# Performance work log

Measured on AMD Instinct MI355X. Metric: run time of the kernel, lower is better.

## Reference

```python
import jax, jax.numpy as jnp
import numpy as np

B = 32768
D_IN = 512      # input_dim == dict_dim (forced by the STE add)
HID = 512       # hard-coded hidden width of linear1
D = 512         # dict_dim / embedding_dim
P = 8           # per_factor_dict_size: number of codebooks / MLP branches
K = 10          # num_factor: codebook size (rows per embedding table)
COMMIT = 0.25


def setup_inputs() -> dict:
    key = jax.random.key(0)
    ks = jax.random.split(key, 7)
    s1 = 1.0 / np.sqrt(D_IN)
    s2 = 1.0 / np.sqrt(HID)
    return {
        "inputs": jax.random.normal(ks[0], (B, D_IN), jnp.float32),
        "W1": jax.random.uniform(ks[1], (P, HID, D_IN), jnp.float32, -s1, s1),
        "b1": jax.random.uniform(ks[2], (P, HID), jnp.float32, -s1, s1),
        "W2": jax.random.uniform(ks[3], (P, D, HID), jnp.float32, -s2, s2),
        "b2": jax.random.uniform(ks[4], (P, D), jnp.float32, -s2, s2),
        # embedding init: uniform(-1/num_factor, 1/num_factor)
        "E": jax.random.uniform(ks[5], (P, K, D), jnp.float32, -1.0 / K, 1.0 / K),
        "label_gen": jax.random.randint(ks[6], (B,), 0, K, jnp.int64),
    }


def reference(inputs, W1, b1, W2, b2, E, label_gen):
    sg = jax.lax.stop_gradient
    # P parallel 2-layer MLPs: [P, B, D]
    h = jax.nn.relu(jnp.einsum("bd,phd->pbh", inputs, W1) + b1[:, None, :])
    z = jnp.einsum("pbh,peh->pbe", h, W2) + b2[:, None, :]
    # squared-distance expansion per codebook: [P, B, K]
    distances = (
        jnp.sum(z * z, axis=-1, keepdims=True)
        + jnp.sum(E * E, axis=-1)[:, None, :]
        - 2.0 * jnp.einsum("pbd,pkd->pbk", z, E)
    )
    ave_distances = jnp.mean(distances, axis=0)          # [B, K]
    idx = jnp.argmin(ave_distances, axis=1)              # [B]
    # one-hot @ E[p] then mean over p == mean codebook gathered at idx
    Emean = jnp.mean(E, axis=0)                          # [K, D]
    vq = Emean[idx]                                      # [B, D]
    vq_z = inputs + sg(vq - inputs)                      # straight-through
    # all_vq_z[j] = mean_p E[p, j]; losses vs every code row: [K, B]
    diff1 = Emean[:, None, :] - sg(inputs)[None, :, :]   # [K, B, D]
    diff2 = sg(Emean)[:, None, :] - inputs[None, :, :]
    all_vq_loss = jnp.sum(diff1 * diff1, axis=-1) + COMMIT * jnp.sum(diff2 * diff2, axis=-1)
    all_vq_z = inputs[None, :, :] + sg(Emean[:, None, :] - inputs[None, :, :])  # [K, B, D]
    changed_vq_z = Emean[label_gen]                      # [B, D]
    return (vq_z, distances, all_vq_z, all_vq_loss, changed_vq_z)
```

## Files before the change

### kernel.cpp

```cpp
#include <hip/hip_runtime.h>
#include <stdint.h>

typedef _Float16 f16;
typedef _Float16 f16x4 __attribute__((ext_vector_type(4)));
typedef _Float16 f16x8 __attribute__((ext_vector_type(8)));
typedef float f32x4 __attribute__((ext_vector_type(4)));

#define B_ROWS 32768
#define DIM 512
#define NP 8
#define NK 10

typedef __attribute__((address_space(3))) unsigned int lds_u32;
typedef __attribute__((address_space(1))) const unsigned int gbl_u32;

__device__ __forceinline__ void gload_lds16(const void* g, void* l) {
  __builtin_amdgcn_global_load_lds((gbl_u32*)(uintptr_t)g, (lds_u32*)(uintptr_t)l, 16, 0, 0);
}


__global__ void prep_split(const float4* __restrict__ X4, f16x4* __restrict__ Xh4,
                           f16x4* __restrict__ Xl4, const float4* __restrict__ W14,
                           f16x4* __restrict__ W1h4, f16x4* __restrict__ W1l4,
                           const float4* __restrict__ W24, f16x4* __restrict__ W2h4) {
  int bid = blockIdx.x, tid = threadIdx.x;
  if (bid < 1024) {
    for (int i = bid * 256 + tid; i < 4194304; i += 1024 * 256) {
      float4 v = X4[i];
      f16x4 h = {(f16)v.x, (f16)v.y, (f16)v.z, (f16)v.w};
      f16x4 l = {(f16)(v.x - (float)h[0]), (f16)(v.y - (float)h[1]),
                 (f16)(v.z - (float)h[2]), (f16)(v.w - (float)h[3])};
      Xh4[i] = h;
      Xl4[i] = l;
    }
  } else if (bid < 1152) {
    for (int i = (bid - 1024) * 256 + tid; i < 524288; i += 128 * 256) {
      float4 v = W14[i];
      f16x4 h = {(f16)v.x, (f16)v.y, (f16)v.z, (f16)v.w};
      f16x4 l = {(f16)(v.x - (float)h[0]), (f16)(v.y - (float)h[1]),
                 (f16)(v.z - (float)h[2]), (f16)(v.w - (float)h[3])};
      W1h4[i] = h;
      W1l4[i] = l;
    }
  } else {
    for (int i = (bid - 1152) * 256 + tid; i < 524288; i += 128 * 256) {
      float4 v = W24[i];
      f16x4 h = {(f16)v.x, (f16)v.y, (f16)v.z, (f16)v.w};
      W2h4[i] = h;
    }
  }
}


__global__ void enorm2(const float* __restrict__ E, float* __restrict__ Emean,
                       float* __restrict__ E2, float* __restrict__ E2m) {
  int bid = blockIdx.x;
  int lane = threadIdx.x;
  if (bid < 80) {
    const float* src = E + (size_t)bid * DIM;
    float s = 0.f;
    for (int i = lane; i < DIM; i += 64) {
      float v = src[i];
      s = fmaf(v, v, s);
    }
#pragma unroll
    for (int m = 1; m < 64; m <<= 1) s += __shfl_xor(s, m, 64);
    if (lane == 0) E2[bid] = s;
  } else {
    int k = bid - 80;
    float acc = 0.f;
    for (int i = lane; i < DIM; i += 64) {
      float s = 0.f;
#pragma unroll
      for (int p = 0; p < NP; ++p) s += E[p * NK * DIM + k * DIM + i];
      s *= 0.125f;
      Emean[k * DIM + i] = s;
      acc = fmaf(s, s, acc);
    }
#pragma unroll
    for (int m = 1; m < 64; m <<= 1) acc += __shfl_xor(acc, m, 64);
    if (lane == 0) E2m[k] = acc;
  }
}


__global__ __launch_bounds__(512) void etilde_kernel(const float* __restrict__ W2,
                                                     const float* __restrict__ b2,
                                                     const float* __restrict__ E,
                                                     f16* __restrict__ EimgH,
                                                     f16* __restrict__ EimgL,
                                                     float* __restrict__ c_) {
  const int p = blockIdx.x / NK, k = blockIdx.x % NK;
  const int h = threadIdx.x;
  __shared__ float Er[512];
  __shared__ float red[8];
  Er[h] = E[((size_t)p * NK + k) * DIM + h];
  __syncthreads();
  const float* Wp = W2 + (size_t)p * DIM * DIM;
  float s = 0.f;
#pragma unroll 8
  for (int d = 0; d < DIM; ++d) s = fmaf(Wp[(size_t)d * DIM + h], Er[d], s);
  int ei = p * 8320 + k * 520 + h;
  f16 hi = (f16)s;
  EimgH[ei] = hi;
  EimgL[ei] = (f16)(s - (float)hi);
  if (h < 8) {
    int pi = p * 8320 + k * 520 + 512 + h;
    EimgH[pi] = (f16)0.f;
    EimgL[pi] = (f16)0.f;
  }
  if (k == 0) {
    for (int j = h; j < 6 * 520; j += 512) {
      int pi = p * 8320 + 10 * 520 + j;
      EimgH[pi] = (f16)0.f;
      EimgL[pi] = (f16)0.f;
    }
  }
  float t = b2[p * DIM + h] * Er[h];
#pragma unroll
  for (int m = 1; m < 64; m <<= 1) t += __shfl_xor(t, m, 64);
  if ((h & 63) == 0) red[h >> 6] = t;
  __syncthreads();
  if (h == 0) {
    float cc = 0.f;
#pragma unroll
    for (int i = 0; i < 8; ++i) cc += red[i];
    c_[p * NK + k] = cc;
  }
}


template <int NBN, int GRP>
__global__ __launch_bounds__(256) void gemm1_k32(
    const f16* __restrict__ Ah_, const f16* __restrict__ Al_,
    const f16* __restrict__ Bh_, const f16* __restrict__ Bl_,
    const float* __restrict__ bias_,
    f16* __restrict__ Oh, f16* __restrict__ Ol, int ldo) {
  __shared__ f16 smem[32768];
  const int tid = threadIdx.x;
  const int lane = tid & 63;
  const int wave = tid >> 6;
  const int wr = wave >> 1, wc = wave & 1;

  const int q8 = gridDim.x >> 3;
  const int bid = blockIdx.x;
  const int swz = (bid & 7) * q8 + (bid >> 3);
  const int band = swz / (GRP * NBN);
  const int r_ = swz % (GRP * NBN);
  const int bm = band * GRP + (r_ % GRP);
  const int bn = r_ / GRP;
  const int m0 = bm * 128, n0 = bn * 128;

  f32x4 acc[4][4] = {};

  auto stage = [&](int buf, int s) {
    int k0 = s * 32;
    f16* base = smem + buf * 16384;
#pragma unroll
    for (int rnd = 0; rnd < 2; ++rnd) {
      int w = rnd * 256 + tid;
      int r = w >> 2;
      int c = ((w & 3) ^ ((r >> 1) & 3)) * 8;
      gload_lds16(Ah_ + (size_t)(m0 + r) * 512 + k0 + c, base + (size_t)w * 8);
      gload_lds16(Al_ + (size_t)(m0 + r) * 512 + k0 + c, base + 4096 + (size_t)w * 8);
      gload_lds16(Bh_ + (size_t)(n0 + r) * 512 + k0 + c, base + 8192 + (size_t)w * 8);
      gload_lds16(Bl_ + (size_t)(n0 + r) * 512 + k0 + c, base + 12288 + (size_t)w * 8);
    }
  };

  stage(0, 0);
  __syncthreads();

  const int g = lane >> 4, rl = lane & 15;

  for (int s = 0; s < 16; ++s) {
    if (s + 1 < 16) stage((s + 1) & 1, s + 1);
    const char* base = (const char*)(smem + (s & 1) * 16384);
    f16x8 af[4][2], bf[4][2];
#pragma unroll
    for (int i = 0; i < 4; ++i) {
      int ra = wr * 64 + i * 16 + rl;
      int offa = ra * 64 + ((g ^ ((ra >> 1) & 3)) << 4);
      af[i][0] = *(const f16x8*)(base + offa);
      af[i][1] = *(const f16x8*)(base + 8192 + offa);
      int rb = wc * 64 + i * 16 + rl;
      int offb = rb * 64 + ((g ^ ((rb >> 1) & 3)) << 4);
      bf[i][0] = *(const f16x8*)(base + 16384 + offb);
      bf[i][1] = *(const f16x8*)(base + 24576 + offb);
    }
#pragma unroll
    for (int i = 0; i < 4; ++i)
#pragma unroll
      for (int jn = 0; jn < 4; ++jn) {
        acc[i][jn] = __builtin_amdgcn_mfma_f32_16x16x32_f16(af[i][0], bf[jn][0], acc[i][jn], 0, 0, 0);
        acc[i][jn] = __builtin_amdgcn_mfma_f32_16x16x32_f16(af[i][0], bf[jn][1], acc[i][jn], 0, 0, 0);
        acc[i][jn] = __builtin_amdgcn_mfma_f32_16x16x32_f16(af[i][1], bf[jn][0], acc[i][jn], 0, 0, 0);
      }
    __syncthreads();
  }

#pragma unroll
  for (int jn = 0; jn < 4; ++jn) {
    int cg = n0 + wc * 64 + jn * 16 + rl;
    float bv = bias_[cg];
#pragma unroll
    for (int i = 0; i < 4; ++i) {
      int r0 = m0 + wr * 64 + i * 16 + g * 4;
#pragma unroll
      for (int r = 0; r < 4; ++r) {
        float z = acc[i][jn][r] + bv;
        z = fmaxf(z, 0.f);
        f16 h = (f16)z;
        size_t off = (size_t)(r0 + r) * ldo + cg;
        Oh[off] = h;
        Ol[off] = (f16)(z - (float)h);
      }
    }
  }
}


__global__ __launch_bounds__(256) void g2d_union(
    const f16* __restrict__ Hh, const f16* __restrict__ Hl,
    const f16* __restrict__ W2h, const float* __restrict__ b2,
    const f16* __restrict__ EimgH, const f16* __restrict__ EimgL,
    const float* __restrict__ c_, float* __restrict__ part2,
    float* __restrict__ gout) {
  __shared__ char pool[66048];
  const int tid = threadIdx.x;
  const int p = blockIdx.y;

  if (blockIdx.x < 1024) {
    f16* smem = (f16*)pool;
    const int lane = tid & 63, wave = tid >> 6;
    const int wr = wave >> 1, wc = wave & 1;
    const int bid = blockIdx.x;
    const int swz = (bid & 7) * 128 + (bid >> 3);
    const int bm = swz >> 2, bn = swz & 3;
    const int m0 = bm * 128, n0 = bn * 128;
    const f16* Ahp = Hh + (size_t)p * 512;
    const f16* Bhp = W2h + (size_t)p * 262144;

    f32x4 acc[4][4] = {};

    auto stage = [&](int buf, int t) {
      int k0 = t * 64;
      f16* sA = smem + buf * 16384;
      f16* sB = sA + 8192;
#pragma unroll
      for (int j = 0; j < 4; ++j) {
        int r = j * 32 + (tid >> 3);
        int c = ((tid & 7) ^ (r & 7)) * 8;
        gload_lds16(Ahp + (size_t)(m0 + r) * 4096 + k0 + c, sA + j * 2048 + tid * 8);
        gload_lds16(Bhp + (size_t)(n0 + r) * 512 + k0 + c, sB + j * 2048 + tid * 8);
      }
    };

    stage(0, 0);
    __syncthreads();
    const int g = lane >> 4, rl = lane & 15;
    for (int s = 0; s < 8; ++s) {
      if (s + 1 < 8) stage((s + 1) & 1, s + 1);
      const char* sA = (const char*)(smem + (s & 1) * 16384);
      const char* sB = sA + 16384;
      f16x8 af[4][2], bf[4][2];
#pragma unroll
      for (int i = 0; i < 4; ++i) {
        int ra = wr * 64 + i * 16 + rl;
        int rb = wc * 64 + i * 16 + rl;
#pragma unroll
        for (int kk = 0; kk < 2; ++kk) {
          int cb = kk * 64 + g * 16;
          af[i][kk] = *(const f16x8*)(sA + ra * 128 + (cb ^ ((ra & 7) << 4)));
          bf[i][kk] = *(const f16x8*)(sB + rb * 128 + (cb ^ ((rb & 7) << 4)));
        }
      }
#pragma unroll
      for (int i = 0; i < 4; ++i)
#pragma unroll
        for (int jn = 0; jn < 4; ++jn)
#pragma unroll
          for (int kk = 0; kk < 2; ++kk)
            acc[i][jn] = __builtin_amdgcn_mfma_f32_16x16x32_f16(af[i][kk], bf[jn][kk], acc[i][jn], 0, 0, 0);
      __syncthreads();
    }

    const float* bp = b2 + (size_t)p * 512;
    float bvals[4];
#pragma unroll
    for (int jn = 0; jn < 4; ++jn) bvals[jn] = bp[n0 + wc * 64 + jn * 16 + rl];
    const int ch = bn * 2 + wc;
    float* pb = part2 + (size_t)(p * 8 + ch) * B_ROWS;
#pragma unroll
    for (int i = 0; i < 4; ++i) {
#pragma unroll
      for (int r = 0; r < 4; ++r) {
        float q = 0.f;
#pragma unroll
        for (int jn = 0; jn < 4; ++jn) {
          float z = acc[i][jn][r] + bvals[jn];
          q = fmaf(z, z, q);
        }
#pragma unroll
        for (int m = 1; m < 16; m <<= 1) q += __shfl_xor(q, m, 64);
        if (rl == 0) pb[m0 + wr * 64 + i * 16 + g * 4 + r] = q;
      }
    }
  } else {
    f16* sH = (f16*)pool;
    f16* sL = (f16*)(pool + 16384);
    f16* sEh = (f16*)(pool + 32768);
    f16* sEl = (f16*)(pool + 49408);
    const int lane = tid & 63, wave = tid >> 6;
    const int r0 = (blockIdx.x - 1024) * 64;
    {
      const uint32_t* ih = (const uint32_t*)(EimgH + (size_t)p * 16 * 520);
      const uint32_t* il = (const uint32_t*)(EimgL + (size_t)p * 16 * 520);
      uint32_t* oh = (uint32_t*)sEh;
      uint32_t* ol = (uint32_t*)sEl;
      for (int i = tid; i < 16 * 520 / 2; i += 256) {
        oh[i] = ih[i];
        ol[i] = il[i];
      }
    }
    const int gq = lane >> 4, rl = lane & 15;

    auto stageT = [&](int buf, int t) {
#pragma unroll
      for (int rnd = 0; rnd < 2; ++rnd) {
        int w = rnd * 256 + tid;
        int r = w >> 3;
        int c = ((w & 7) ^ (r & 7)) * 8;
        gload_lds16(Hh + (size_t)(r0 + r) * 4096 + p * DIM + t * 64 + c,
                    sH + buf * 4096 + (size_t)w * 8);
        gload_lds16(Hl + (size_t)(r0 + r) * 4096 + p * DIM + t * 64 + c,
                    sL + buf * 4096 + (size_t)w * 8);
      }
    };

    f32x4 acc = {};
    stageT(0, 0);
    __syncthreads();

    for (int t = 0; t < 8; ++t) {
      if (t < 7) stageT((t + 1) & 1, t + 1);
      const char* bh = (const char*)(sH + (t & 1) * 4096);
      const char* bl = (const char*)(sL + (t & 1) * 4096);
      const int ra = wave * 16 + rl;
      f16x8 ah[2], al[2], beh[2], bel[2];
#pragma unroll
      for (int kk = 0; kk < 2; ++kk) {
        int cb = kk * 64 + gq * 16;
        ah[kk] = *(const f16x8*)(bh + ra * 128 + (cb ^ ((ra & 7) << 4)));
        al[kk] = *(const f16x8*)(bl + ra * 128 + (cb ^ ((ra & 7) << 4)));
        int ce = t * 128 + kk * 64 + gq * 16;
        beh[kk] = *(const f16x8*)((const char*)sEh + rl * 1040 + ce);
        bel[kk] = *(const f16x8*)((const char*)sEl + rl * 1040 + ce);
      }
#pragma unroll
      for (int kk = 0; kk < 2; ++kk) {
        acc = __builtin_amdgcn_mfma_f32_16x16x32_f16(ah[kk], beh[kk], acc, 0, 0, 0);
        acc = __builtin_amdgcn_mfma_f32_16x16x32_f16(ah[kk], bel[kk], acc, 0, 0, 0);
        acc = __builtin_amdgcn_mfma_f32_16x16x32_f16(al[kk], beh[kk], acc, 0, 0, 0);
      }
      __syncthreads();
    }
    if (rl < NK) {
      float cv = c_[p * NK + rl];
#pragma unroll
      for (int r = 0; r < 4; ++r) {
        int row = r0 + wave * 16 + gq * 4 + r;
        gout[((size_t)p * B_ROWS + row) * NK + rl] = acc[r] + cv;
      }
    }
  }
}


__global__ __launch_bounds__(256) void final_kernel(
    const float* __restrict__ X, const float* __restrict__ part2,
    float* __restrict__ gdist, const float* __restrict__ E2,
    const float* __restrict__ Emean, const float* __restrict__ E2m,
    const int* __restrict__ label, float* __restrict__ vq_z,
    float* __restrict__ avz, float* __restrict__ loss, float* __restrict__ changed) {
  __shared__ float Em[NK * DIM];
  __shared__ float e2s[NK];
  const int tid = threadIdx.x;
  for (int i = tid; i < NK * DIM; i += 256) Em[i] = Emean[i];
  if (tid < NK) e2s[tid] = E2m[tid];
  __syncthreads();

  const int b0 = blockIdx.x * 16;
  {
    const float4* Em4 = (const float4*)Em;
    float4* avz4 = (float4*)avz;
    if (blockIdx.x < 256) {
      for (int it = 0; it < 80; ++it) {
        int idx = it * 256 + tid;
        int d4 = idx & 127, row = (idx >> 7) & 15, k = idx >> 11;
        if (k == 8) continue;
        avz4[(((size_t)k * B_ROWS + b0 + row) << 7) + d4] = Em4[k * 128 + d4];
      }
    } else {
      for (int it = 0; it < 80; ++it) {
        int idx = it * 256 + tid;
        int d4 = idx & 127, row = (idx >> 7) & 15, k = idx >> 11;
        avz4[(((size_t)k * B_ROWS + b0 + row) << 7) + d4] = Em4[k * 128 + d4];
      }
    }
  }

  const int lane = tid & 63, wave = tid >> 6;
  const int pl = lane & 7, kh = lane >> 3;
  for (int rr = 0; rr < 4; ++rr) {
    int b = b0 + wave * 4 + rr;
    float zq = part2[(size_t)(pl * 8 + kh) * B_ROWS + b];
    zq += __shfl_xor(zq, 8, 64);
    zq += __shfl_xor(zq, 16, 64);
    zq += __shfl_xor(zq, 32, 64);
    float g0 = gdist[((size_t)pl * B_ROWS + b) * NK + kh];
    float g1 = (lane < 16) ? gdist[((size_t)pl * B_ROWS + b) * NK + 8 + kh] : 0.f;
    float dv0 = zq + E2[pl * NK + kh] - 2.f * g0;
    float dv1 = zq + E2[pl * NK + 8 + kh] - 2.f * g1;
    gdist[((size_t)pl * B_ROWS + b) * NK + kh] = dv0;
    if (lane < 16) gdist[((size_t)pl * B_ROWS + b) * NK + 8 + kh] = dv1;
    float v0 = dv0, v1 = (lane < 16) ? dv1 : 0.f;
#pragma unroll
    for (int m = 1; m < 8; m <<= 1) {
      v0 += __shfl_xor(v0, m, 64);
      v1 += __shfl_xor(v1, m, 64);
    }
    float a[NK];
#pragma unroll
    for (int k = 0; k < 8; ++k) a[k] = __shfl(v0, k * 8, 64);
    a[8] = __shfl(v1, 0, 64);
    a[9] = __shfl(v1, 8, 64);
    int idx = 0;
    float mn = a[0];
#pragma unroll
    for (int k = 1; k < NK; ++k) {
      if (a[k] < mn) { mn = a[k]; idx = k; }
    }
    const float* xr = X + (size_t)b * DIM;
    float sx = 0.f, dx[NK] = {};
#pragma unroll
    for (int j = 0; j < 8; ++j) {
      float x = xr[j * 64 + lane];
      sx = fmaf(x, x, sx);
#pragma unroll
      for (int k = 0; k < NK; ++k) dx[k] = fmaf(x, Em[k * DIM + j * 64 + lane], dx[k]);
    }
#pragma unroll
    for (int m = 1; m < 64; m <<= 1) {
      sx += __shfl_xor(sx, m, 64);
#pragma unroll
      for (int k = 0; k < NK; ++k) dx[k] += __shfl_xor(dx[k], m, 64);
    }
    if (lane == 0) {
#pragma unroll
      for (int k = 0; k < NK; ++k)
        loss[(size_t)k * B_ROWS + b] = 1.25f * (sx - 2.f * dx[k] + e2s[k]);
    }
    int lab = label[b];
#pragma unroll
    for (int j = 0; j < 8; ++j) {
      int c = j * 64 + lane;
      vq_z[(size_t)b * DIM + c] = Em[idx * DIM + c];
      changed[(size_t)b * DIM + c] = Em[lab * DIM + c];
    }
  }
}


__global__ void bcast_rest(const float* __restrict__ Emean, float4* __restrict__ avz4) {
  const float4* Em4 = (const float4*)Emean;
  int tid = blockIdx.x * 256 + threadIdx.x;
  for (int it = 0; it < 32; ++it) {
    int idx = tid + it * 16384;
    int b = idx >> 7, d4 = idx & 127;
    avz4[((size_t)(8 * B_ROWS + b) << 7) + d4] = Em4[8 * 128 + d4];
  }
}


extern "C" void kernel_launch(void* const* d_in, const int* in_sizes, int n_in,
                              void* d_out, int out_size, void* d_ws, size_t ws_size,
                              hipStream_t stream) {
  const float* X = (const float*)d_in[0];
  const float* W1 = (const float*)d_in[1];
  const float* b1 = (const float*)d_in[2];
  const float* W2 = (const float*)d_in[3];
  const float* b2 = (const float*)d_in[4];
  const float* E = (const float*)d_in[5];
  const int* lab = (const int*)d_in[6];
  float* out = (float*)d_out;

  float* vq_z = out;
  float* dist = out + 16777216;
  float* avz = out + 16777216 + 2621440;
  float* loss = avz + 167772160;
  float* chg = loss + 327680;

  f16* Xh = (f16*)vq_z;
  f16* Xl = Xh + 16777216;
  f16* Hh = (f16*)avz;
  f16* Hl = Hh + 134217728;
  float* part2 = avz + 134217728;

  char* w = (char*)d_ws;
  f16* W1h = (f16*)w; w += 4194304;
  f16* W1l = (f16*)w; w += 4194304;
  f16* W2h = (f16*)w; w += 4194304;
  float* Emean = (float*)w; w += NK * DIM * 4;
  float* E2 = (float*)w; w += 512;
  float* E2m = (float*)w; w += 256;
  float* c_ = (float*)w; w += 512;
  f16* EimgH = (f16*)w; w += NP * 16 * 520 * 2;
  f16* EimgL = (f16*)w; w += NP * 16 * 520 * 2;

  prep_split<<<1280, 256, 0, stream>>>((const float4*)X, (f16x4*)Xh, (f16x4*)Xl,
                                       (const float4*)W1, (f16x4*)W1h, (f16x4*)W1l,
                                       (const float4*)W2, (f16x4*)W2h);
  enorm2<<<90, 64, 0, stream>>>(E, Emean, E2, E2m);
  etilde_kernel<<<80, 512, 0, stream>>>(W2, b2, E, EimgH, EimgL, c_);

  gemm1_k32<32, 8><<<dim3(8192, 1, 1), 256, 0, stream>>>(
      Xh, Xl, W1h, W1l, b1, Hh, Hl, 4096);

  g2d_union<<<dim3(1536, NP), 256, 0, stream>>>(Hh, Hl, W2h, b2, EimgH, EimgL, c_,
                                                part2, dist);

  final_kernel<<<2048, 256, 0, stream>>>(X, part2, dist, E2, Emean, E2m, lab,
                                         vq_z, avz, loss, chg);
  bcast_rest<<<64, 256, 0, stream>>>(Emean, (float4*)avz);
}
```

Measured before the change: 1.085 ms.

## Split batch in halves and overlap second-half GEMM1 with first-half GEMM2/dots

The first GEMM is split into two batch halves. The second half's GEMM1 tiles are interleaved in one launch with the first half's GEMM2 and codebook-dot blocks, and a third launch finishes the second half's GEMM2 and dots. The goal is to fill the tail and idle time between dependent kernels by mixing compute-heavy and lighter blocks. The cost is a larger LDS footprint for GEMM1 blocks inside the mega kernel, which may reduce occupancy, plus changed block swizzles that affect cache locality.

```diff
diff --git a/kernel.cpp b/kernel.cpp
--- a/kernel.cpp
+++ b/kernel.cpp
@@ -130,25 +130,15 @@
 }
 
 
-template <int NBN, int GRP>
-__global__ __launch_bounds__(256) void gemm1_k32(
+__device__ __forceinline__ void gemm1_body(
+    char* pool, int tid, int bm, int bn,
     const f16* __restrict__ Ah_, const f16* __restrict__ Al_,
     const f16* __restrict__ Bh_, const f16* __restrict__ Bl_,
-    const float* __restrict__ bias_,
-    f16* __restrict__ Oh, f16* __restrict__ Ol, int ldo) {
-  __shared__ f16 smem[32768];
-  const int tid = threadIdx.x;
+    const float* __restrict__ bias_, f16* __restrict__ Oh, f16* __restrict__ Ol) {
+  f16* smem = (f16*)pool;
   const int lane = tid & 63;
   const int wave = tid >> 6;
   const int wr = wave >> 1, wc = wave & 1;
-
-  const int q8 = gridDim.x >> 3;
-  const int bid = blockIdx.x;
-  const int swz = (bid & 7) * q8 + (bid >> 3);
-  const int band = swz / (GRP * NBN);
-  const int r_ = swz % (GRP * NBN);
-  const int bm = band * GRP + (r_ % GRP);
-  const int bn = r_ / GRP;
   const int m0 = bm * 128, n0 = bn * 128;
 
   f32x4 acc[4][4] = {};
@@ -211,7 +201,7 @@
         float z = acc[i][jn][r] + bv;
         z = fmaxf(z, 0.f);
         f16 h = (f16)z;
-        size_t off = (size_t)(r0 + r) * ldo + cg;
+        size_t off = (size_t)(r0 + r) * 4096 + cg;
         Oh[off] = h;
         Ol[off] = (f16)(z - (float)h);
       }
@@ -219,160 +209,214 @@
   }
 }
 
-
-__global__ __launch_bounds__(256) void g2d_union(
+__device__ __forceinline__ void gemm2_body(
+    char* pool, int tid, int p, int bm, int bn,
+    const f16* __restrict__ Hh, const f16* __restrict__ W2h,
+    const float* __restrict__ b2, float* __restrict__ part2) {
+  f16* smem = (f16*)pool;
+  const int lane = tid & 63, wave = tid >> 6;
+  const int wr = wave >> 1, wc = wave & 1;
+  const int m0 = bm * 128, n0 = bn * 128;
+  const f16* Ahp = Hh + (size_t)p * 512;
+  const f16* Bhp = W2h + (size_t)p * 262144;
+
+  f32x4 acc[4][4] = {};
+
+  auto stage = [&](int buf, int t) {
+    int k0 = t * 64;
+    f16* sA = smem + buf * 16384;
+    f16* sB = sA + 8192;
+#pragma unroll
+    for (int j = 0; j < 4; ++j) {
+      int r = j * 32 + (tid >> 3);
+      int c = ((tid & 7) ^ (r & 7)) * 8;
+      gload_lds16(Ahp + (size_t)(m0 + r) * 4096 + k0 + c, sA + j * 2048 + tid * 8);
+      gload_lds16(Bhp + (size_t)(n0 + r) * 512 + k0 + c, sB + j * 2048 + tid * 8);
+    }
+  };
+
+  stage(0, 0);
+  __syncthreads();
+  const int g = lane >> 4, rl = lane & 15;
+  for (int s = 0; s < 8; ++s) {
+    if (s + 1 < 8) stage((s + 1) & 1, s + 1);
+    const char* sA = (const char*)(smem + (s & 1) * 16384);
+    const char* sB = sA + 16384;
+    f16x8 af[4][2], bf[4][2];
+#pragma unroll
+    for (int i = 0; i < 4; ++i) {
+      int ra = wr * 64 + i * 16 + rl;
+      int rb = wc * 64 + i * 16 + rl;
+#pragma unroll
+      for (int kk = 0; kk < 2; ++kk) {
+        int cb = kk * 64 + g * 16;
+        af[i][kk] = *(const f16x8*)(sA + ra * 128 + (cb ^ ((ra & 7) << 4)));
+        bf[i][kk] = *(const f16x8*)(sB + rb * 128 + (cb ^ ((rb & 7) << 4)));
+      }
+    }
+#pragma unroll
+    for (int i = 0; i < 4; ++i)
+#pragma unroll
+      for (int jn = 0; jn < 4; ++jn)
+#pragma unroll
+        for (int kk = 0; kk < 2; ++kk)
+          acc[i][jn] = __builtin_amdgcn_mfma_f32_16x16x32_f16(af[i][kk], bf[jn][kk], acc[i][jn], 0, 0, 0);
+    __syncthreads();
+  }
+
+  const float* bp = b2 + (size_t)p * 512;
+  float bvals[4];
+#pragma unroll
+  for (int jn = 0; jn < 4; ++jn) bvals[jn] = bp[n0 + wc * 64 + jn * 16 + rl];
+  const int ch = bn * 2 + wc;
+  float* pb = part2 + (size_t)(p * 8 + ch) * B_ROWS;
+#pragma unroll
+  for (int i = 0; i < 4; ++i) {
+#pragma unroll
+    for (int r = 0; r < 4; ++r) {
+      float q = 0.f;
+#pragma unroll
+      for (int jn = 0; jn < 4; ++jn) {
+        float z = acc[i][jn][r] + bvals[jn];
+        q = fmaf(z, z, q);
+      }
+#pragma unroll
+      for (int m = 1; m < 16; m <<= 1) q += __shfl_xor(q, m, 64);
+      if (rl == 0) pb[m0 + wr * 64 + i * 16 + g * 4 + r] = q;
+    }
+  }
+}
+
+__device__ __forceinline__ void dots_body(
+    char* pool, int tid, int p, int r0,
+    const f16* __restrict__ Hh, const f16* __restrict__ Hl,
+    const f16* __restrict__ EimgH, const f16* __restrict__ EimgL,
+    const float* __restrict__ c_, float* __restrict__ gout) {
+  f16* sH = (f16*)pool;
+  f16* sL = (f16*)(pool + 16384);
+  f16* sEh = (f16*)(pool + 32768);
+  f16* sEl = (f16*)(pool + 49408);
+  const int lane = tid & 63, wave = tid >> 6;
+  {
+    const uint32_t* ih = (const uint32_t*)(EimgH + (size_t)p * 16 * 520);
+    const uint32_t* il = (const uint32_t*)(EimgL + (size_t)p * 16 * 520);
+    uint32_t* oh = (uint32_t*)sEh;
+    uint32_t* ol = (uint32_t*)sEl;
+    for (int i = tid; i < 16 * 520 / 2; i += 256) {
+      oh[i] = ih[i];
+      ol[i] = il[i];
+    }
+  }
+  const int gq = lane >> 4, rl = lane & 15;
+
+  auto stageT = [&](int buf, int t) {
+#pragma unroll
+    for (int rnd = 0; rnd < 2; ++rnd) {
+      int w = rnd * 256 + tid;
+      int r = w >> 3;
+      int c = ((w & 7) ^ (r & 7)) * 8;
+      gload_lds16(Hh + (size_t)(r0 + r) * 4096 + p * DIM + t * 64 + c,
+                  sH + buf * 4096 + (size_t)w * 8);
+      gload_lds16(Hl + (size_t)(r0 + r) * 4096 + p * DIM + t * 64 + c,
+                  sL + buf * 4096 + (size_t)w * 8);
+    }
+  };
+
+  f32x4 acc = {};
+  stageT(0, 0);
+  __syncthreads();
+
+  for (int t = 0; t < 8; ++t) {
+    if (t < 7) stageT((t + 1) & 1, t + 1);
+    const char* bh = (const char*)(sH + (t & 1) * 4096);
+    const char* bl = (const char*)(sL + (t & 1) * 4096);
+    const int ra = wave * 16 + rl;
+    f16x8 ah[2], al[2], beh[2], bel[2];
+#pragma unroll
+    for (int kk = 0; kk < 2; ++kk) {
+      int cb = kk * 64 + gq * 16;
+      ah[kk] = *(const f16x8*)(bh + ra * 128 + (cb ^ ((ra & 7) << 4)));
+      al[kk] = *(const f16x8*)(bl + ra * 128 + (cb ^ ((ra & 7) << 4)));
+      int ce = t * 128 + kk * 64 + gq * 16;
+      beh[kk] = *(const f16x8*)((const char*)sEh + rl * 1040 + ce);
+      bel[kk] = *(const f16x8*)((const char*)sEl + rl * 1040 + ce);
+    }
+#pragma unroll
+    for (int kk = 0; kk < 2; ++kk) {
+      acc = __builtin_amdgcn_mfma_f32_16x16x32_f16(ah[kk], beh[kk], acc, 0, 0, 0);
+      acc = __builtin_amdgcn_mfma_f32_16x16x32_f16(ah[kk], bel[kk], acc, 0, 0, 0);
+      acc = __builtin_amdgcn_mfma_f32_16x16x32_f16(al[kk], beh[kk], acc, 0, 0, 0);
+    }
+    __syncthreads();
+  }
+  if (rl < NK) {
+    float cv = c_[p * NK + rl];
+#pragma unroll
+    for (int r = 0; r < 4; ++r) {
+      int row = r0 + wave * 16 + gq * 4 + r;
+      gout[((size_t)p * B_ROWS + row) * NK + rl] = acc[r] + cv;
+    }
+  }
+}
+
+
+__global__ __launch_bounds__(256) void gemm1_half(
+    int bmbase, const f16* __restrict__ Ah_, const f16* __restrict__ Al_,
+    const f16* __restrict__ Bh_, const f16* __restrict__ Bl_,
+    const float* __restrict__ bias_, f16* __restrict__ Oh, f16* __restrict__ Ol) {
+  __shared__ char pool[65536];
+  const int x = blockIdx.x;
+  const int swz = (x & 7) * 512 + (x >> 3);
+  const int band = swz >> 8, r_ = swz & 255;
+  gemm1_body(pool, threadIdx.x, bmbase + band * 8 + (r_ & 7), r_ >> 3,
+             Ah_, Al_, Bh_, Bl_, bias_, Oh, Ol);
+}
+
+__global__ __launch_bounds__(256) void mega_k2(
+    const f16* __restrict__ Xh, const f16* __restrict__ Xl,
+    const f16* __restrict__ W1h, const f16* __restrict__ W1l,
+    const float* __restrict__ b1, f16* __restrict__ Hh, f16* __restrict__ Hl,
+    const f16* __restrict__ W2h, const float* __restrict__ b2,
+    const f16* __restrict__ EimgH, const f16* __restrict__ EimgL,
+    const float* __restrict__ c_, float* __restrict__ part2,
+    float* __restrict__ gout) {
+  __shared__ char pool[66048];
+  const int x = blockIdx.x;
+  const int slot = x % 5, grp = x / 5;
+  const int tid = threadIdx.x;
+  if (slot < 2) {
+    int idx = grp * 2 + slot;
+    int swz = (idx & 7) * 512 + (idx >> 3);
+    int band = swz >> 8, r_ = swz & 255;
+    gemm1_body(pool, tid, 128 + band * 8 + (r_ & 7), r_ >> 3,
+               Xh, Xl, W1h, W1l, b1, Hh, Hl);
+  } else if (slot < 4) {
+    int idx = grp * 2 + (slot - 2);
+    int p = idx >> 9, j = idx & 511;
+    int swz = (j & 7) * 64 + (j >> 3);
+    gemm2_body(pool, tid, p, swz >> 2, swz & 3, Hh, W2h, b2, part2);
+  } else {
+    int p = grp >> 8, j = grp & 255;
+    dots_body(pool, tid, p, j * 64, Hh, Hl, EimgH, EimgL, c_, gout);
+  }
+}
+
+__global__ __launch_bounds__(256) void mega_k3(
     const f16* __restrict__ Hh, const f16* __restrict__ Hl,
     const f16* __restrict__ W2h, const float* __restrict__ b2,
     const f16* __restrict__ EimgH, const f16* __restrict__ EimgL,
     const float* __restrict__ c_, float* __restrict__ part2,
     float* __restrict__ gout) {
   __shared__ char pool[66048];
+  const int x = blockIdx.x;
   const int tid = threadIdx.x;
-  const int p = blockIdx.y;
-
-  if (blockIdx.x < 1024) {
-    f16* smem = (f16*)pool;
-    const int lane = tid & 63, wave = tid >> 6;
-    const int wr = wave >> 1, wc = wave & 1;
-    const int bid = blockIdx.x;
-    const int swz = (bid & 7) * 128 + (bid >> 3);
-    const int bm = swz >> 2, bn = swz & 3;
-    const int m0 = bm * 128, n0 = bn * 128;
-    const f16* Ahp = Hh + (size_t)p * 512;
-    const f16* Bhp = W2h + (size_t)p * 262144;
-
-    f32x4 acc[4][4] = {};
-
-    auto stage = [&](int buf, int t) {
-      int k0 = t * 64;
-      f16* sA = smem + buf * 16384;
-      f16* sB = sA + 8192;
-#pragma unroll
-      for (int j = 0; j < 4; ++j) {
-        int r = j * 32 + (tid >> 3);
-        int c = ((tid & 7) ^ (r & 7)) * 8;
-        gload_lds16(Ahp + (size_t)(m0 + r) * 4096 + k0 + c, sA + j * 2048 + tid * 8);
-        gload_lds16(Bhp + (size_t)(n0 + r) * 512 + k0 + c, sB + j * 2048 + tid * 8);
-      }
-    };
-
-    stage(0, 0);
-    __syncthreads();
-    const int g = lane >> 4, rl = lane & 15;
-    for (int s = 0; s < 8; ++s) {
-      if (s + 1 < 8) stage((s + 1) & 1, s + 1);
-      const char* sA = (const char*)(smem + (s & 1) * 16384);
-      const char* sB = sA + 16384;
-      f16x8 af[4][2], bf[4][2];
-#pragma unroll
-      for (int i = 0; i < 4; ++i) {
-        int ra = wr * 64 + i * 16 + rl;
-        int rb = wc * 64 + i * 16 + rl;
-#pragma unroll
-        for (int kk = 0; kk < 2; ++kk) {
-          int cb = kk * 64 + g * 16;
-          af[i][kk] = *(const f16x8*)(sA + ra * 128 + (cb ^ ((ra & 7) << 4)));
-          bf[i][kk] = *(const f16x8*)(sB + rb * 128 + (cb ^ ((rb & 7) << 4)));
-        }
-      }
-#pragma unroll
-      for (int i = 0; i < 4; ++i)
-#pragma unroll
-        for (int jn = 0; jn < 4; ++jn)
-#pragma unroll
-          for (int kk = 0; kk < 2; ++kk)
-            acc[i][jn] = __builtin_amdgcn_mfma_f32_16x16x32_f16(af[i][kk], bf[jn][kk], acc[i][jn], 0, 0, 0);
-      __syncthreads();
-    }
-
-    const float* bp = b2 + (size_t)p * 512;
-    float bvals[4];
-#pragma unroll
-    for (int jn = 0; jn < 4; ++jn) bvals[jn] = bp[n0 + wc * 64 + jn * 16 + rl];
-    const int ch = bn * 2 + wc;
-    float* pb = part2 + (size_t)(p * 8 + ch) * B_ROWS;
-#pragma unroll
-    for (int i = 0; i < 4; ++i) {
-#pragma unroll
-      for (int r = 0; r < 4; ++r) {
-        float q = 0.f;
-#pragma unroll
-        for (int jn = 0; jn < 4; ++jn) {
-          float z = acc[i][jn][r] + bvals[jn];
-          q = fmaf(z, z, q);
-        }
-#pragma unroll
-        for (int m = 1; m < 16; m <<= 1) q += __shfl_xor(q, m, 64);
-        if (rl == 0) pb[m0 + wr * 64 + i * 16 + g * 4 + r] = q;
-      }
-    }
+  if (x < 4096) {
+    int p = x >> 9, j = x & 511;
+    int swz = (j & 7) * 64 + (j >> 3);
+    gemm2_body(pool, tid, p, 128 + (swz >> 2), swz & 3, Hh, W2h, b2, part2);
   } else {
-    f16* sH = (f16*)pool;
-    f16* sL = (f16*)(pool + 16384);
-    f16* sEh = (f16*)(pool + 32768);
-    f16* sEl = (f16*)(pool + 49408);
-    const int lane = tid & 63, wave = tid >> 6;
-    const int r0 = (blockIdx.x - 1024) * 64;
-    {
-      const uint32_t* ih = (const uint32_t*)(EimgH + (size_t)p * 16 * 520);
-      const uint32_t* il = (const uint32_t*)(EimgL + (size_t)p * 16 * 520);
-      uint32_t* oh = (uint32_t*)sEh;
-      uint32_t* ol = (uint32_t*)sEl;
-      for (int i = tid; i < 16 * 520 / 2; i += 256) {
-        oh[i] = ih[i];
-        ol[i] = il[i];
-      }
-    }
-    const int gq = lane >> 4, rl = lane & 15;
-
-    auto stageT = [&](int buf, int t) {
-#pragma unroll
-      for (int rnd = 0; rnd < 2; ++rnd) {
-        int w = rnd * 256 + tid;
-        int r = w >> 3;
-        int c = ((w & 7) ^ (r & 7)) * 8;
-        gload_lds16(Hh + (size_t)(r0 + r) * 4096 + p * DIM + t * 64 + c,
-                    sH + buf * 4096 + (size_t)w * 8);
-        gload_lds16(Hl + (size_t)(r0 + r) * 4096 + p * DIM + t * 64 + c,
-                    sL + buf * 4096 + (size_t)w * 8);
-      }
-    };
-
-    f32x4 acc = {};
-    stageT(0, 0);
-    __syncthreads();
-
-    for (int t = 0; t < 8; ++t) {
-      if (t < 7) stageT((t + 1) & 1, t + 1);
-      const char* bh = (const char*)(sH + (t & 1) * 4096);
-      const char* bl = (const char*)(sL + (t & 1) * 4096);
-      const int ra = wave * 16 + rl;
-      f16x8 ah[2], al[2], beh[2], bel[2];
-#pragma unroll
-      for (int kk = 0; kk < 2; ++kk) {
-        int cb = kk * 64 + gq * 16;
-        ah[kk] = *(const f16x8*)(bh + ra * 128 + (cb ^ ((ra & 7) << 4)));
-        al[kk] = *(const f16x8*)(bl + ra * 128 + (cb ^ ((ra & 7) << 4)));
-        int ce = t * 128 + kk * 64 + gq * 16;
-        beh[kk] = *(const f16x8*)((const char*)sEh + rl * 1040 + ce);
-        bel[kk] = *(const f16x8*)((const char*)sEl + rl * 1040 + ce);
-      }
-#pragma unroll
-      for (int kk = 0; kk < 2; ++kk) {
-        acc = __builtin_amdgcn_mfma_f32_16x16x32_f16(ah[kk], beh[kk], acc, 0, 0, 0);
-        acc = __builtin_amdgcn_mfma_f32_16x16x32_f16(ah[kk], bel[kk], acc, 0, 0, 0);
-        acc = __builtin_amdgcn_mfma_f32_16x16x32_f16(al[kk], beh[kk], acc, 0, 0, 0);
-      }
-      __syncthreads();
-    }
-    if (rl < NK) {
-      float cv = c_[p * NK + rl];
-#pragma unroll
-      for (int r = 0; r < 4; ++r) {
-        int row = r0 + wave * 16 + gq * 4 + r;
-        gout[((size_t)p * B_ROWS + row) * NK + rl] = acc[r] + cv;
-      }
-    }
+    int i = x - 4096;
+    dots_body(pool, tid, i >> 8, 16384 + (i & 255) * 64, Hh, Hl, EimgH, EimgL, c_, gout);
   }
 }
 
@@ -524,11 +568,10 @@
   enorm2<<<90, 64, 0, stream>>>(E, Emean, E2, E2m);
   etilde_kernel<<<80, 512, 0, stream>>>(W2, b2, E, EimgH, EimgL, c_);
 
-  gemm1_k32<32, 8><<<dim3(8192, 1, 1), 256, 0, stream>>>(
-      Xh, Xl, W1h, W1l, b1, Hh, Hl, 4096);
-
-  g2d_union<<<dim3(1536, NP), 256, 0, stream>>>(Hh, Hl, W2h, b2, EimgH, EimgL, c_,
-                                                part2, dist);
+  gemm1_half<<<4096, 256, 0, stream>>>(0, Xh, Xl, W1h, W1l, b1, Hh, Hl);
+  mega_k2<<<10240, 256, 0, stream>>>(Xh, Xl, W1h, W1l, b1, Hh, Hl, W2h, b2,
+                                     EimgH, EimgL, c_, part2, dist);
+  mega_k3<<<6144, 256, 0, stream>>>(Hh, Hl, W2h, b2, EimgH, EimgL, c_, part2, dist);
 
   final_kernel<<<2048, 256, 0, stream>>>(X, part2, dist, E2, Emean, E2m, lab,
                                          vq_z, avz, loss, chg);
```

After: 1.095 ms. No clear change (+0.9%).
